# Kernel optimization log

Hardware: AMD Instinct MI355X
Metric: run time of the kernel (lower is better)

The kernel has to match this reference:

```python
import jax, jax.numpy as jnp
import numpy as np

B, S, HE, HD = 32, 2048, 1024, 1024

def setup_inputs() -> dict:
    key = jax.random.key(0)
    k1, k2, k3, k4, k5 = jax.random.split(key, 5)
    enc_hiddens = jax.random.normal(k1, (B, S, HE), dtype=jnp.float32)
    dec_hidden = jax.random.normal(k2, (B, HD), dtype=jnp.float32)
    mask = jax.random.randint(k3, (B, S), 0, 2).astype(bool)  # True = masked out
    # params init uniform(-0.05, 0.05) as in init_weights
    W = jax.random.uniform(k4, (HD, HE + HD), dtype=jnp.float32, minval=-0.05, maxval=0.05)
    V = jax.random.uniform(k5, (1, HD), dtype=jnp.float32, minval=-0.05, maxval=0.05)
    return {"enc_hiddens": enc_hiddens, "dec_hidden": dec_hidden, "mask": mask, "W": W, "V": V}

def reference(enc_hiddens, dec_hidden, mask, W, V):
    # e = V^T tanh(W [enc; dec]) -- split W to avoid materializing the concat:
    # W @ [enc;dec] == W_enc @ enc + W_dec @ dec (same math, fused-friendly)
    HE_ = enc_hiddens.shape[-1]
    W_enc, W_dec = W[:, :HE_], W[:, HE_:]
    h = jnp.tanh(jnp.einsum('bse,de->bsd', enc_hiddens, W_enc)
                 + jnp.einsum('be,de->bd', dec_hidden, W_dec)[:, None, :])  # [B,S,HD]
    scores = jnp.einsum('bsd,od->bs', h, V)  # [B,S] (o==1 squeezed)
    scores = jnp.where(mask, -jnp.inf, scores)
    attn = jax.nn.softmax(scores, axis=1)[:, None, :]  # [B,1,S]
    ctx = jnp.einsum('bos,bse->be', attn, enc_hiddens)  # squeeze of bmm -> [B,HE]
    return (ctx, attn)
```

## Files before the change

### kernel.cpp

```cpp
#include <hip/hip_runtime.h>
#include <hip/hip_bf16.h>
#include <math.h>

#define BB 32
#define SS 2048
#define HE 1024
#define HD 1024
#define WROW (HE + HD)

typedef __attribute__((ext_vector_type(8))) short bf16x8;
typedef __attribute__((ext_vector_type(4))) float f32x4;
typedef __attribute__((ext_vector_type(8))) unsigned short u16x8;

__device__ __forceinline__ unsigned short f2bf(float f) {
    union { float f; unsigned u; } v; v.f = f;
    unsigned r = v.u + 0x7fffu + ((v.u >> 16) & 1u);
    return (unsigned short)(r >> 16);
}

__device__ __forceinline__ unsigned int pk2(float x, float y) {
    union { __hip_bfloat162 h; unsigned int u; } c;
    c.h = __float22bfloat162_rn(float2{x, y});
    return c.u;
}

#define LGKM0()  asm volatile("s_waitcnt lgkmcnt(0)" ::: "memory")
#define BAR()    asm volatile("s_barrier" ::: "memory")

__global__ __launch_bounds__(256) void k_cvt_wfrag(const float* __restrict__ W,
                                                   unsigned short* __restrict__ wf) {
    int i = blockIdx.x * 256 + threadIdx.x;
    int d = i >> 7;
    int c = i & 127;
    const float4* src = (const float4*)(W + (size_t)d * WROW + c * 8);
    float4 a = src[0], b2 = src[1];
    u16x8 o;
    o[0] = f2bf(a.x);  o[1] = f2bf(a.y);  o[2] = f2bf(a.z);  o[3] = f2bf(a.w);
    o[4] = f2bf(b2.x); o[5] = f2bf(b2.y); o[6] = f2bf(b2.z); o[7] = f2bf(b2.w);
    int ksg = c >> 2, hi = c & 3;
    int l   = (d & 15) + 16 * hi;
    int g   = d >> 4;
    *(u16x8*)(wf + ((size_t)(g * 32 + ksg) * 64 + l) * 8) = o;
}

__global__ __launch_bounds__(256) void k_projdec2(const float* __restrict__ dec,
                                                  const float* __restrict__ W,
                                                  float* __restrict__ proj) {
    const int tid = threadIdx.x;
    const int dl = tid >> 6;
    const int b  = (tid >> 1) & 31;
    const int hf = tid & 1;
    const int d  = blockIdx.x * 4 + dl;
    const float* wrow = W + (size_t)d * WROW + HE + hf * 512;
    const float* dv   = dec + b * HD + hf * 512;
    float s = 0.f;
    #pragma unroll 4
    for (int e = 0; e < 512; e += 4) {
        float4 w4 = *(const float4*)(wrow + e);
        float4 x4 = *(const float4*)(dv + e);
        s += w4.x * x4.x + w4.y * x4.y + w4.z * x4.z + w4.w * x4.w;
    }
    s += __shfl_xor(s, 1, 64);
    if (hf == 0) proj[b * HD + d] = s;
}

__global__ __launch_bounds__(512, 2) void k_scores_mfma8b(
        const float* __restrict__ enc,
        const unsigned short* __restrict__ wf,
        const float* __restrict__ V,
        const float* __restrict__ proj,
        float* __restrict__ psc) {
    __shared__ unsigned short SM[16384];

    const int tid = threadIdx.x;
    const int wv = tid >> 6, ln = tid & 63, l15 = ln & 15, lg = ln >> 4;

    const int lid  = (blockIdx.x & 7) * 128 + (blockIdx.x >> 3);
    const int t0   = lid * 64;
    const int b    = t0 >> 11;

    f32x4 acc[4][8];
    #pragma unroll
    for (int m = 0; m < 4; m++)
        #pragma unroll
        for (int n = 0; n < 8; n++) acc[m][n] = (f32x4){0.f, 0.f, 0.f, 0.f};

    float4 areg[2];
    bf16x8 bgA[4], bgB[4], bgC[4], bgD[4];

    #define LOAD_A(k) do { \
        const float4* g_ = (const float4*)(enc + (size_t)(t0 + (tid >> 3)) * 1024 + (k) + (tid & 7) * 8); \
        areg[0] = g_[0]; areg[1] = g_[1]; \
    } while (0)

    #define CVTW_A(buf) do { \
        int row_ = tid >> 3; \
        union { u16x8 s; uint4 u; } pk_; \
        pk_.u.x = pk2(areg[0].x, areg[0].y); \
        pk_.u.y = pk2(areg[0].z, areg[0].w); \
        pk_.u.z = pk2(areg[1].x, areg[1].y); \
        pk_.u.w = pk2(areg[1].z, areg[1].w); \
        *(u16x8*)&SM[(buf) * 4096 + row_ * 64 + (((tid & 7) ^ (row_ & 7)) << 3)] = pk_.s; \
    } while (0)

    #define LOADB(bgx, tt, ksl, no) do { \
        _Pragma("unroll") \
        for (int n = 0; n < 4; n++) { \
            int g_ = wv * 8 + (no) + n; \
            bgx[n] = *(const bf16x8*)(wf + ((size_t)(g_ * 32 + (tt) * 2 + (ksl)) * 64 + ln) * 8); \
        } } while (0)

    #define RD_A(af, Ac, ks) do { \
        _Pragma("unroll") \
        for (int m = 0; m < 4; m++) { \
            int row_ = m * 16 + l15; \
            af[m] = *(const bf16x8*)&(Ac)[row_ * 64 + ((((ks) + lg) ^ (row_ & 7)) << 3)]; \
        } } while (0)

    #define MFMA4N(no, bg, af) do { \
        __builtin_amdgcn_s_setprio(1); \
        _Pragma("unroll") \
        for (int m = 0; m < 4; m++) \
            _Pragma("unroll") \
            for (int n = 0; n < 4; n++) \
                acc[m][(no) + n] = __builtin_amdgcn_mfma_f32_16x16x32_bf16(af[m], bg[n], acc[m][(no) + n], 0, 0, 0); \
        __builtin_amdgcn_s_setprio(0); } while (0)

    LOADB(bgA, 0, 0, 0); LOADB(bgB, 0, 0, 4);
    LOADB(bgC, 0, 1, 0); LOADB(bgD, 0, 1, 4);
    LOAD_A(0);
    CVTW_A(0);
    LOAD_A(64);
    LGKM0(); BAR();

    for (int t = 0; t < 16; ++t) {
        const int cur = t & 1, nxt = cur ^ 1;
        const unsigned short* Ac = SM + cur * 4096;
        bf16x8 af[4];

        RD_A(af, Ac, 0);
        MFMA4N(0, bgA, af);
        MFMA4N(4, bgB, af);

        if (t < 15) {
            LOADB(bgA, t + 1, 0, 0);
            LOADB(bgB, t + 1, 0, 4);
            CVTW_A(nxt);
            if (t < 14) LOAD_A((t + 2) * 64);
        }

        RD_A(af, Ac, 4);
        MFMA4N(0, bgC, af);
        MFMA4N(4, bgD, af);

        if (t < 15) {
            LOADB(bgC, t + 1, 1, 0);
            LOADB(bgD, t + 1, 1, 4);
            LGKM0(); BAR();
        }
    }
    #undef LOAD_A
    #undef CVTW_A
    #undef LOADB
    #undef RD_A
    #undef MFMA4N

    float sc[4][4];
    #pragma unroll
    for (int m = 0; m < 4; m++)
        #pragma unroll
        for (int j = 0; j < 4; j++) sc[m][j] = 0.f;
    #pragma unroll
    for (int n = 0; n < 8; n++) {
        int d = wv * 128 + n * 16 + l15;
        float pd  = proj[b * 1024 + d];
        float vv  = V[d];
        float vv2 = 2.f * vv;
        #pragma unroll
        for (int m = 0; m < 4; m++)
            #pragma unroll
            for (int j = 0; j < 4; j++) {
                float y  = acc[m][n][j] + pd;
                float e2 = __expf(2.f * y);
                float r  = __builtin_amdgcn_rcpf(e2 + 1.f);
                sc[m][j] += vv - vv2 * r;
            }
    }

    __syncthreads();
    float* red = (float*)SM;
    #pragma unroll
    for (int m = 0; m < 4; m++)
        #pragma unroll
        for (int j = 0; j < 4; j++) {
            int tok = m * 16 + lg * 4 + j;
            int col = wv * 16 + l15;
            red[tok * 128 + ((col + tok) & 127)] = sc[m][j];
        }
    __syncthreads();
    if (tid < 64) {
        float s = 0.f;
        #pragma unroll
        for (int x = 0; x < 128; x++) s += red[tid * 128 + ((x + tid) & 127)];
        psc[t0 + tid] = s;
    }
}

__global__ __launch_bounds__(256) void k_softmax_p(const float* __restrict__ psc,
                                                   const int* __restrict__ mask,
                                                   float* __restrict__ attn) {
    __shared__ float sred[256];
    const int b = blockIdx.x, tid = threadIdx.x;
    float vals[8];
    int   msk[8];
    float lmax = -1e30f;
    #pragma unroll
    for (int i = 0; i < 8; i++) {
        int s = tid + i * 256;
        vals[i] = psc[b * SS + s];
        msk[i]  = mask[b * SS + s];
        if (!msk[i]) lmax = fmaxf(lmax, vals[i]);
    }
    sred[tid] = lmax; __syncthreads();
    for (int off = 128; off > 0; off >>= 1) {
        if (tid < off) sred[tid] = fmaxf(sred[tid], sred[tid + off]);
        __syncthreads();
    }
    float m = sred[0];
    __syncthreads();
    float ex[8];
    float lsum = 0.f;
    #pragma unroll
    for (int i = 0; i < 8; i++) {
        ex[i] = msk[i] ? 0.f : __expf(vals[i] - m);
        lsum += ex[i];
    }
    sred[tid] = lsum; __syncthreads();
    for (int off = 128; off > 0; off >>= 1) {
        if (tid < off) sred[tid] += sred[tid + off];
        __syncthreads();
    }
    float inv = 1.f / sred[0];
    #pragma unroll
    for (int i = 0; i < 8; i++) attn[b * SS + tid + i * 256] = ex[i] * inv;
}

__global__ __launch_bounds__(256) void k_ctx_part(const float* __restrict__ enc,
                                                  const float* __restrict__ attn,
                                                  float* __restrict__ pctx) {
    const int b = blockIdx.x, z = blockIdx.y, tid = threadIdx.x;
    float4 acc = {0.f, 0.f, 0.f, 0.f};
    const float4* e4 = (const float4*)(enc + ((size_t)b * SS + z * 64) * HE);
    const float*  ar = attn + b * SS + z * 64;
    for (int s = 0; s < 64; s++) {
        float a = ar[s];
        if (a != 0.f) {
            float4 v = e4[(size_t)s * 256 + tid];
            acc.x += a * v.x; acc.y += a * v.y; acc.z += a * v.z; acc.w += a * v.w;
        }
    }
    *(float4*)(pctx + ((size_t)z * 32 + b) * 1024 + tid * 4) = acc;
}

__global__ __launch_bounds__(256) void k_ctx_red(const float* __restrict__ pctx,
                                                 float* __restrict__ ctx) {
    int i = blockIdx.x * 256 + threadIdx.x;
    float s = 0.f;
    #pragma unroll
    for (int z = 0; z < 32; z++) s += pctx[z * 32768 + i];
    ctx[i] = s;
}

__global__ __launch_bounds__(256) void k_scores_f32(const float* __restrict__ enc,
                                                    const float* __restrict__ W,
                                                    const float* __restrict__ V,
                                                    const float* __restrict__ proj,
                                                    float* __restrict__ scores) {
    __shared__ float As[64][20];
    __shared__ float Bs[64][20];
    __shared__ float red[64][17];
    const int t0 = blockIdx.x * 64;
    const int b  = t0 >> 11;
    const int tid = threadIdx.x;
    const int tx = tid & 15, ty = tid >> 4;
    const int lrow = tid >> 2, lc4 = (tid & 3) * 4;
    float sc[4] = {0.f, 0.f, 0.f, 0.f};
    for (int n0 = 0; n0 < HD; n0 += 64) {
        float C[4][4] = {};
        for (int k0 = 0; k0 < HE; k0 += 16) {
            *(float4*)&As[lrow][lc4] = *(const float4*)(enc + (size_t)(t0 + lrow) * HE + k0 + lc4);
            *(float4*)&Bs[lrow][lc4] = *(const float4*)(W + (size_t)(n0 + lrow) * WROW + k0 + lc4);
            __syncthreads();
            #pragma unroll
            for (int k4 = 0; k4 < 16; k4 += 4) {
                float4 a[4], bb[4];
                #pragma unroll
                for (int i = 0; i < 4; i++) a[i]  = *(float4*)&As[ty * 4 + i][k4];
                #pragma unroll
                for (int j = 0; j < 4; j++) bb[j] = *(float4*)&Bs[tx * 4 + j][k4];
                #pragma unroll
                for (int i = 0; i < 4; i++)
                    #pragma unroll
                    for (int j = 0; j < 4; j++)
                        C[i][j] += a[i].x * bb[j].x + a[i].y * bb[j].y +
                                   a[i].z * bb[j].z + a[i].w * bb[j].w;
            }
            __syncthreads();
        }
        #pragma unroll
        for (int j = 0; j < 4; j++) {
            int d = n0 + tx * 4 + j;
            float pd = proj[b * HD + d];
            float v  = V[d];
            #pragma unroll
            for (int i = 0; i < 4; i++) {
                float y  = C[i][j] + pd;
                float e2 = __expf(2.f * y);
                sc[i] += v * (1.f - 2.f / (e2 + 1.f));
            }
        }
    }
    #pragma unroll
    for (int i = 0; i < 4; i++) red[ty * 4 + i][tx] = sc[i];
    __syncthreads();
    if (tid < 64) {
        float s = 0.f;
        #pragma unroll
        for (int x = 0; x < 16; x++) s += red[tid][x];
        scores[t0 + tid] = s;
    }
}

__global__ __launch_bounds__(256) void k_softmax_f32(float* __restrict__ sc_attn,
                                                     const int* __restrict__ mask) {
    __shared__ float sred[256];
    const int b = blockIdx.x, tid = threadIdx.x;
    float vals[8]; int msk[8];
    float lmax = -1e30f;
    #pragma unroll
    for (int i = 0; i < 8; i++) {
        int s = tid + i * 256;
        vals[i] = sc_attn[b * SS + s];
        msk[i]  = mask[b * SS + s];
        if (!msk[i]) lmax = fmaxf(lmax, vals[i]);
    }
    sred[tid] = lmax; __syncthreads();
    for (int off = 128; off > 0; off >>= 1) {
        if (tid < off) sred[tid] = fmaxf(sred[tid], sred[tid + off]);
        __syncthreads();
    }
    float m = sred[0];
    __syncthreads();
    float ex[8]; float lsum = 0.f;
    #pragma unroll
    for (int i = 0; i < 8; i++) { ex[i] = msk[i] ? 0.f : __expf(vals[i] - m); lsum += ex[i]; }
    sred[tid] = lsum; __syncthreads();
    for (int off = 128; off > 0; off >>= 1) {
        if (tid < off) sred[tid] += sred[tid + off];
        __syncthreads();
    }
    float inv = 1.f / sred[0];
    #pragma unroll
    for (int i = 0; i < 8; i++) sc_attn[b * SS + tid + i * 256] = ex[i] * inv;
}

__global__ __launch_bounds__(256) void k_ctx_atomic(const float* __restrict__ enc,
                                                    const float* __restrict__ attn,
                                                    float* __restrict__ ctx) {
    const int b = blockIdx.x;
    const int e = blockIdx.y * 256 + threadIdx.x;
    const int s0 = blockIdx.z * 256;
    float sum = 0.f;
    for (int s = s0; s < s0 + 256; s++)
        sum += attn[b * SS + s] * enc[((size_t)b * SS + s) * HE + e];
    atomicAdd(&ctx[b * HE + e], sum);
}

extern "C" void kernel_launch(void* const* d_in, const int* in_sizes, int n_in,
                              void* d_out, int out_size, void* d_ws, size_t ws_size,
                              hipStream_t stream) {
    const float* enc  = (const float*)d_in[0];
    const float* dec  = (const float*)d_in[1];
    const int*   mask = (const int*)d_in[2];
    const float* W    = (const float*)d_in[3];
    const float* V    = (const float*)d_in[4];

    float* out  = (float*)d_out;
    float* ctx  = out;
    float* attn = out + BB * HE;

    const size_t WF_OFF = 0, PROJ_OFF = 2097152, PSC_OFF = PROJ_OFF + 131072,
                 PCTX_OFF = PSC_OFF + 1048576, WS_NEED = PCTX_OFF + 4194304;
    if (ws_size >= WS_NEED) {
        char* w = (char*)d_ws;
        unsigned short* wf = (unsigned short*)(w + WF_OFF);
        float* proj        = (float*)(w + PROJ_OFF);
        float* psc         = (float*)(w + PSC_OFF);
        float* pctx        = (float*)(w + PCTX_OFF);

        k_cvt_wfrag<<<512, 256, 0, stream>>>(W, wf);
        k_projdec2<<<256, 256, 0, stream>>>(dec, W, proj);
        k_scores_mfma8b<<<1024, 512, 0, stream>>>(enc, wf, V, proj, psc);
        k_softmax_p<<<BB, 256, 0, stream>>>(psc, mask, attn);
        k_ctx_part<<<dim3(BB, 32), 256, 0, stream>>>(enc, attn, pctx);
        k_ctx_red<<<128, 256, 0, stream>>>(pctx, ctx);
    } else {
        float* proj  = ctx;
        float* score = attn;
        k_projdec2<<<256, 256, 0, stream>>>(dec, W, proj);
        k_scores_f32<<<(BB * SS) / 64, 256, 0, stream>>>(enc, W, V, proj, score);
        k_softmax_f32<<<BB, 256, 0, stream>>>(score, mask);
        hipMemsetAsync(ctx, 0, (size_t)BB * HE * sizeof(float), stream);
        k_ctx_atomic<<<dim3(BB, HE / 256, 8), 256, 0, stream>>>(enc, attn, ctx);
    }
}
```

Baseline: 204.7 us.

## Switch score GEMM to 32x32x16 MFMA with matching weight fragment layout

Replaces the 16x16x32 bf16 MFMA tiling with 32x32x16 MFMAs. The pre-converted W fragment layout is reordered to match, accumulators become 2x4 f32x16 tiles, and the LDS A-fragment reads are remapped. The epilogue now reduces scores across the 32 columns with wavefront shuffles before a much smaller LDS reduction, and the shared buffer is halved. The larger MFMA shape is meant to reduce LDS fragment reads and instruction count per FLOP. The cost is more register pressure and a new lane-to-token mapping that has to be correct.

Measured after the change: 221.8 us. 8.3% more time.

```diff
diff --git a/kernel.cpp b/kernel.cpp
--- a/kernel.cpp
+++ b/kernel.cpp
@@ -10,6 +10,7 @@
 
 typedef __attribute__((ext_vector_type(8))) short bf16x8;
 typedef __attribute__((ext_vector_type(4))) float f32x4;
+typedef __attribute__((ext_vector_type(16))) float f32x16;
 typedef __attribute__((ext_vector_type(8))) unsigned short u16x8;
 
 __device__ __forceinline__ unsigned short f2bf(float f) {
@@ -37,10 +38,10 @@
     u16x8 o;
     o[0] = f2bf(a.x);  o[1] = f2bf(a.y);  o[2] = f2bf(a.z);  o[3] = f2bf(a.w);
     o[4] = f2bf(b2.x); o[5] = f2bf(b2.y); o[6] = f2bf(b2.z); o[7] = f2bf(b2.w);
-    int ksg = c >> 2, hi = c & 3;
-    int l   = (d & 15) + 16 * hi;
-    int g   = d >> 4;
-    *(u16x8*)(wf + ((size_t)(g * 32 + ksg) * 64 + l) * 8) = o;
+    int ks = c >> 1;
+    int l  = (d & 31) + 32 * (c & 1);
+    int g  = d >> 5;
+    *(u16x8*)(wf + ((size_t)(g * 64 + ks) * 64 + l) * 8) = o;
 }
 
 __global__ __launch_bounds__(256) void k_projdec2(const float* __restrict__ dec,
@@ -70,23 +71,25 @@
         const float* __restrict__ V,
         const float* __restrict__ proj,
         float* __restrict__ psc) {
-    __shared__ unsigned short SM[16384];
+    __shared__ unsigned short SM[8192];
 
     const int tid = threadIdx.x;
-    const int wv = tid >> 6, ln = tid & 63, l15 = ln & 15, lg = ln >> 4;
+    const int wv = tid >> 6, ln = tid & 63, l31 = ln & 31, hi = ln >> 5;
 
     const int lid  = (blockIdx.x & 7) * 128 + (blockIdx.x >> 3);
     const int t0   = lid * 64;
     const int b    = t0 >> 11;
 
-    f32x4 acc[4][8];
-    #pragma unroll
-    for (int m = 0; m < 4; m++)
-        #pragma unroll
-        for (int n = 0; n < 8; n++) acc[m][n] = (f32x4){0.f, 0.f, 0.f, 0.f};
+    f32x16 acc[2][4];
+    #pragma unroll
+    for (int m = 0; m < 2; m++)
+        #pragma unroll
+        for (int n = 0; n < 4; n++)
+            #pragma unroll
+            for (int r = 0; r < 16; r++) acc[m][n][r] = 0.f;
 
     float4 areg[2];
-    bf16x8 bgA[4], bgB[4], bgC[4], bgD[4];
+    bf16x8 bgE[8], bgF[8];
 
     #define LOAD_A(k) do { \
         const float4* g_ = (const float4*)(enc + (size_t)(t0 + (tid >> 3)) * 1024 + (k) + (tid & 7) * 8); \
@@ -103,31 +106,33 @@
         *(u16x8*)&SM[(buf) * 4096 + row_ * 64 + (((tid & 7) ^ (row_ & 7)) << 3)] = pk_.s; \
     } while (0)
 
-    #define LOADB(bgx, tt, ksl, no) do { \
+    #define LOADB(bgx, tt, ksb) do { \
         _Pragma("unroll") \
-        for (int n = 0; n < 4; n++) { \
-            int g_ = wv * 8 + (no) + n; \
-            bgx[n] = *(const bf16x8*)(wf + ((size_t)(g_ * 32 + (tt) * 2 + (ksl)) * 64 + ln) * 8); \
-        } } while (0)
-
-    #define RD_A(af, Ac, ks) do { \
-        _Pragma("unroll") \
-        for (int m = 0; m < 4; m++) { \
-            int row_ = m * 16 + l15; \
-            af[m] = *(const bf16x8*)&(Ac)[row_ * 64 + ((((ks) + lg) ^ (row_ & 7)) << 3)]; \
-        } } while (0)
-
-    #define MFMA4N(no, bg, af) do { \
-        __builtin_amdgcn_s_setprio(1); \
-        _Pragma("unroll") \
-        for (int m = 0; m < 4; m++) \
+        for (int kk = 0; kk < 2; kk++) \
             _Pragma("unroll") \
             for (int n = 0; n < 4; n++) \
-                acc[m][(no) + n] = __builtin_amdgcn_mfma_f32_16x16x32_bf16(af[m], bg[n], acc[m][(no) + n], 0, 0, 0); \
-        __builtin_amdgcn_s_setprio(0); } while (0)
-
-    LOADB(bgA, 0, 0, 0); LOADB(bgB, 0, 0, 4);
-    LOADB(bgC, 0, 1, 0); LOADB(bgD, 0, 1, 4);
+                bgx[kk * 4 + n] = *(const bf16x8*)(wf + ((size_t)((wv * 4 + n) * 64 + (tt) * 4 + (ksb) + kk) * 64 + ln) * 8); \
+        } while (0)
+
+    #define HALF(bg, ksb, Ac) do { \
+        _Pragma("unroll") \
+        for (int kk = 0; kk < 2; kk++) { \
+            bf16x8 af0, af1; \
+            { int c_ = ((ksb) + kk) * 2 + hi; int row_ = l31; \
+              af0 = *(const bf16x8*)&(Ac)[row_ * 64 + ((c_ ^ (row_ & 7)) << 3)]; } \
+            { int c_ = ((ksb) + kk) * 2 + hi; int row_ = 32 + l31; \
+              af1 = *(const bf16x8*)&(Ac)[row_ * 64 + ((c_ ^ (row_ & 7)) << 3)]; } \
+            __builtin_amdgcn_s_setprio(1); \
+            _Pragma("unroll") \
+            for (int n = 0; n < 4; n++) \
+                acc[0][n] = __builtin_amdgcn_mfma_f32_32x32x16_bf16(af0, bg[kk * 4 + n], acc[0][n], 0, 0, 0); \
+            _Pragma("unroll") \
+            for (int n = 0; n < 4; n++) \
+                acc[1][n] = __builtin_amdgcn_mfma_f32_32x32x16_bf16(af1, bg[kk * 4 + n], acc[1][n], 0, 0, 0); \
+            __builtin_amdgcn_s_setprio(0); \
+        } } while (0)
+
+    LOADB(bgE, 0, 0); LOADB(bgF, 0, 2);
     LOAD_A(0);
     CVTW_A(0);
     LOAD_A(64);
@@ -136,72 +141,78 @@
     for (int t = 0; t < 16; ++t) {
         const int cur = t & 1, nxt = cur ^ 1;
         const unsigned short* Ac = SM + cur * 4096;
-        bf16x8 af[4];
-
-        RD_A(af, Ac, 0);
-        MFMA4N(0, bgA, af);
-        MFMA4N(4, bgB, af);
+
+        HALF(bgE, 0, Ac);
 
         if (t < 15) {
-            LOADB(bgA, t + 1, 0, 0);
-            LOADB(bgB, t + 1, 0, 4);
+            LOADB(bgE, t + 1, 0);
             CVTW_A(nxt);
             if (t < 14) LOAD_A((t + 2) * 64);
         }
 
-        RD_A(af, Ac, 4);
-        MFMA4N(0, bgC, af);
-        MFMA4N(4, bgD, af);
+        HALF(bgF, 2, Ac);
 
         if (t < 15) {
-            LOADB(bgC, t + 1, 1, 0);
-            LOADB(bgD, t + 1, 1, 4);
+            LOADB(bgF, t + 1, 2);
             LGKM0(); BAR();
         }
     }
     #undef LOAD_A
     #undef CVTW_A
     #undef LOADB
-    #undef RD_A
-    #undef MFMA4N
-
-    float sc[4][4];
-    #pragma unroll
-    for (int m = 0; m < 4; m++)
-        #pragma unroll
-        for (int j = 0; j < 4; j++) sc[m][j] = 0.f;
-    #pragma unroll
-    for (int n = 0; n < 8; n++) {
-        int d = wv * 128 + n * 16 + l15;
+    #undef HALF
+
+    float sc[2][16];
+    #pragma unroll
+    for (int m = 0; m < 2; m++)
+        #pragma unroll
+        for (int r = 0; r < 16; r++) sc[m][r] = 0.f;
+    #pragma unroll
+    for (int n = 0; n < 4; n++) {
+        int d = wv * 128 + n * 32 + l31;
         float pd  = proj[b * 1024 + d];
         float vv  = V[d];
         float vv2 = 2.f * vv;
         #pragma unroll
-        for (int m = 0; m < 4; m++)
+        for (int m = 0; m < 2; m++)
             #pragma unroll
-            for (int j = 0; j < 4; j++) {
-                float y  = acc[m][n][j] + pd;
+            for (int r = 0; r < 16; r++) {
+                float y  = acc[m][n][r] + pd;
                 float e2 = __expf(2.f * y);
-                float r  = __builtin_amdgcn_rcpf(e2 + 1.f);
-                sc[m][j] += vv - vv2 * r;
+                float rc = __builtin_amdgcn_rcpf(e2 + 1.f);
+                sc[m][r] += vv - vv2 * rc;
             }
     }
 
+    #pragma unroll
+    for (int m = 0; m < 2; m++)
+        #pragma unroll
+        for (int r = 0; r < 16; r++) {
+            float v = sc[m][r];
+            v += __shfl_xor(v, 1, 64);
+            v += __shfl_xor(v, 2, 64);
+            v += __shfl_xor(v, 4, 64);
+            v += __shfl_xor(v, 8, 64);
+            v += __shfl_xor(v, 16, 64);
+            sc[m][r] = v;
+        }
+
     __syncthreads();
-    float* red = (float*)SM;
-    #pragma unroll
-    for (int m = 0; m < 4; m++)
-        #pragma unroll
-        for (int j = 0; j < 4; j++) {
-            int tok = m * 16 + lg * 4 + j;
-            int col = wv * 16 + l15;
-            red[tok * 128 + ((col + tok) & 127)] = sc[m][j];
-        }
+    float* redf = (float*)SM;
+    if (l31 == 0) {
+        #pragma unroll
+        for (int m = 0; m < 2; m++)
+            #pragma unroll
+            for (int r = 0; r < 16; r++) {
+                int tok = m * 32 + (r & 3) + 8 * (r >> 2) + 4 * hi;
+                redf[tok * 8 + wv] = sc[m][r];
+            }
+    }
     __syncthreads();
     if (tid < 64) {
         float s = 0.f;
         #pragma unroll
-        for (int x = 0; x < 128; x++) s += red[tid * 128 + ((x + tid) & 127)];
+        for (int w = 0; w < 8; w++) s += redf[tid * 8 + w];
         psc[t0 + tid] = s;
     }
 }
```
